# Kernel tuning notes

Hardware: AMD Instinct MI355X
Metric: run time of the kernel (lower is better)

The kernel has to match this reference:

```python
import jax, jax.numpy as jnp
import numpy as np

EPS = 1e-5
NUM_GROUPS = 32


def group_norm(x, scale, bias):
    # x: [B, C, H, W]; normalize over (C//G, H, W) within each of G groups
    B, C, H, W = x.shape
    g = x.reshape(B, NUM_GROUPS, C // NUM_GROUPS, H, W)
    mean = g.mean(axis=(2, 3, 4), keepdims=True)
    var = g.var(axis=(2, 3, 4), keepdims=True)
    g = (g - mean) * jax.lax.rsqrt(var + EPS)
    g = g.reshape(B, C, H, W)
    return g * scale[None, :, None, None] + bias[None, :, None, None]


def conv1x1(x, w, b):
    # x: [B, C, H, W], w: [Cout, Cin], b: [Cout]
    return jnp.einsum('bchw,oc->bohw', x, w) + b[None, :, None, None]


def setup_inputs() -> dict:
    key = jax.random.key(0)
    ks = jax.random.split(key, 8)
    B, C, H, W = 8, 256, 64, 64
    xavier = (6.0 / (C + C)) ** 0.5
    inp = {
        'x': jax.random.normal(ks[0], (B, C, H, W), jnp.float32),
        'target': jax.random.normal(ks[1], (B, C, H, W), jnp.float32),
        'gn_scale': jnp.ones((C,), jnp.float32),
        'gn_bias': jnp.zeros((C,), jnp.float32),
        'Wq': jax.random.uniform(ks[2], (C, C), jnp.float32, -xavier, xavier),
        'bq': jnp.zeros((C,), jnp.float32),
        'Wk': jax.random.uniform(ks[3], (C, C), jnp.float32, -xavier, xavier),
        'bk': jnp.zeros((C,), jnp.float32),
        'Wv': jax.random.uniform(ks[4], (C, C), jnp.float32, -xavier, xavier),
        'bv': jnp.zeros((C,), jnp.float32),
        'Wp': jax.random.uniform(ks[5], (C, C), jnp.float32, -xavier, xavier) * 1e-05,
        'bp': jnp.zeros((C,), jnp.float32),
    }
    return inp


def reference(x, target, gn_scale, gn_bias, Wq, bq, Wk, bk, Wv, bv, Wp, bp):
    B, C, H, W = x.shape
    hx = group_norm(x, gn_scale, gn_bias)
    hy = group_norm(target, gn_scale, gn_bias)
    q = conv1x1(hx, Wq, bq)  # [B,C,H,W]
    k = conv1x1(hy, Wk, bk)
    v = conv1x1(hy, Wv, bv)
    q = q.transpose(0, 2, 3, 1).reshape(B, H * W, C)  # [B,HW,C]
    k = k.reshape(B, C, H * W)                         # [B,C,HW]
    w = jnp.einsum('bnc,bcm->bnm', q, k) * (C ** -0.5)  # [B,HW,HW]
    w = jax.nn.softmax(w, axis=-1)
    v = v.transpose(0, 2, 3, 1).reshape(B, H * W, C)   # [B,HW,C]
    h = jnp.einsum('bnm,bmc->bnc', w, v)               # [B,HW,C]
    h = h.reshape(B, H, W, C).transpose(0, 3, 1, 2)    # [B,C,H,W]
    return conv1x1(h, Wp, bp)
```

## Files before the change

### kernel.cpp

```cpp
#include <hip/hip_runtime.h>
#include <cstdint>
#include <cstddef>

typedef _Float16 f16;
typedef _Float16 half8 __attribute__((ext_vector_type(8)));
typedef float floatx4 __attribute__((ext_vector_type(4)));

#define B_ 8
#define C_ 256
#define HW_ 4096
#define EPS_ 1e-5f
#define KVB 32
#define DEFER_THR 8.0f
#define WP_S 65536.0f
#define WP_I (1.0f / 65536.0f)

__device__ __forceinline__ floatx4 mfma16(half8 a, half8 b, floatx4 c) {
  return __builtin_amdgcn_mfma_f32_16x16x32_f16(a, b, c, 0, 0, 0);
}

__global__ void gn_stats(const float* __restrict__ x, const float* __restrict__ y,
                         float* __restrict__ stats) {
  int bid = blockIdx.x;
  int which = bid >> 8;
  int b = (bid >> 5) & 7;
  int g = bid & 31;
  const float* src = which ? y : x;
  const float* base = src + ((size_t)b * C_ + (size_t)g * 8) * HW_;
  float s = 0.f, ss = 0.f;
  const float4* base4 = (const float4*)base;
  for (int i = threadIdx.x; i < 8 * HW_ / 4; i += 256) {
    float4 v = base4[i];
    s += v.x + v.y + v.z + v.w;
    ss += v.x * v.x + v.y * v.y + v.z * v.z + v.w * v.w;
  }
#pragma unroll
  for (int m = 1; m <= 32; m <<= 1) { s += __shfl_xor(s, m); ss += __shfl_xor(ss, m); }
  __shared__ float red[8];
  int wv = threadIdx.x >> 6;
  if ((threadIdx.x & 63) == 0) { red[wv] = s; red[4 + wv] = ss; }
  __syncthreads();
  if (threadIdx.x == 0) {
    float S = red[0] + red[1] + red[2] + red[3];
    float SS = red[4] + red[5] + red[6] + red[7];
    float mean = S / 32768.f;
    float var = SS / 32768.f - mean * mean;
    stats[bid * 2 + 0] = mean;
    stats[bid * 2 + 1] = rsqrtf(var + EPS_);
  }
}

__global__ void gn_apply(const float* __restrict__ x, const float* __restrict__ y,
                         const float* __restrict__ stats,
                         const float* __restrict__ gsc, const float* __restrict__ gbi,
                         f16* __restrict__ hx, f16* __restrict__ hy) {
  int bid = blockIdx.x;
  int which = bid >> 10;
  int b = (bid >> 7) & 7;
  int hw0 = (bid & 127) * 32;
  const float* src = which ? y : x;
  f16* dst = which ? hy : hx;
  const float* st = stats + which * (B_ * 32 * 2);
  int hw = threadIdx.x & 31;
  int c0 = (threadIdx.x >> 5) * 32;
  uint4 ob[4];
  f16* buf = (f16*)ob;
#pragma unroll
  for (int cc = 0; cc < 32; ++cc) {
    int c = c0 + cc;
    int g = c >> 3;
    float mean = st[(b * 32 + g) * 2 + 0];
    float rstd = st[(b * 32 + g) * 2 + 1];
    float v = src[((size_t)b * C_ + c) * HW_ + hw0 + hw];
    v = (v - mean) * rstd * gsc[c] + gbi[c];
    buf[cc] = (f16)v;
  }
  uint4* o4 = (uint4*)(dst + ((size_t)b * HW_ + hw0 + hw) * C_ + c0);
  o4[0] = ob[0]; o4[1] = ob[1]; o4[2] = ob[2]; o4[3] = ob[3];
}

__global__ void w2h(const float* __restrict__ wq, const float* __restrict__ wk,
                    const float* __restrict__ wv, const float* __restrict__ wp,
                    f16* __restrict__ o) {
  int i = blockIdx.x * 256 + threadIdx.x;
  int m = i >> 16, r = i & 65535;
  float v = (m == 0) ? wq[r] : (m == 1) ? wk[r] : (m == 2) ? wv[r] : wp[r] * WP_S;
  o[i] = (f16)v;
}

template<int BIASM, int OUT>
__global__ __launch_bounds__(256, 2) void gemmh(
    const f16* __restrict__ A, const f16* __restrict__ Bp,
    const float* __restrict__ bias, void* __restrict__ Cout,
    int N, float alpha, long sA, long sB, long sC) {
  __shared__ f16 at[64][264];
  __shared__ f16 bt[64][264];
  int z = blockIdx.z;
  const f16* Ab = A + (size_t)z * sA;
  const f16* Bb = Bp + (size_t)z * sB;
  int bm = blockIdx.x * 64, bn = blockIdx.y * 64;
  int t = threadIdx.x;
  int lane = t & 63, wv = t >> 6, l15 = lane & 15, koff = (lane >> 4) * 8;
  {
    int row = t >> 2, c0 = (t & 3) * 64;
    const uint4* pa = (const uint4*)(Ab + (size_t)(bm + row) * 256 + c0);
    const uint4* pb = (const uint4*)(Bb + (size_t)(bn + row) * 256 + c0);
    uint4* da = (uint4*)&at[row][c0];
    uint4* db = (uint4*)&bt[row][c0];
#pragma unroll
    for (int u = 0; u < 8; ++u) da[u] = pa[u];
#pragma unroll
    for (int u = 0; u < 8; ++u) db[u] = pb[u];
  }
  __syncthreads();
  floatx4 acc[4];
#pragma unroll
  for (int nt = 0; nt < 4; ++nt) acc[nt] = (floatx4){0.f, 0.f, 0.f, 0.f};
#pragma unroll
  for (int kk = 0; kk < 256; kk += 32) {
    half8 a = *(const half8*)&at[wv * 16 + l15][kk + koff];
#pragma unroll
    for (int nt = 0; nt < 4; ++nt) {
      half8 b = *(const half8*)&bt[nt * 16 + l15][kk + koff];
      acc[nt] = mfma16(a, b, acc[nt]);
    }
  }
#pragma unroll
  for (int nt = 0; nt < 4; ++nt) {
    int n = bn + nt * 16 + l15;
#pragma unroll
    for (int r = 0; r < 4; ++r) {
      int m = bm + wv * 16 + (lane >> 4) * 4 + r;
      float bv = bias[BIASM ? m : n];
      size_t idx = (size_t)z * sC + (size_t)m * N + n;
      if (OUT == 0) ((float*)Cout)[idx] = acc[nt][r] * alpha + bv;
      else          ((f16*)Cout)[idx] = (f16)((acc[nt][r] + bv) * alpha);
    }
  }
}

__global__ __launch_bounds__(512, 1) void flashf(
    const f16* __restrict__ Q, const f16* __restrict__ K,
    const f16* __restrict__ V, f16* __restrict__ Hh) {
  int flat = blockIdx.x;
  int b = flat & 7;
  int m0 = (flat >> 3) * 128;
  int t = threadIdx.x;
  int lane = t & 63;
  int wv = t >> 6;
  int l15 = lane & 15;
  int koff = (lane >> 4) * 8;
  const f16* Qb = Q + (size_t)b * HW_ * C_;
  const f16* Kb = K + (size_t)b * HW_ * C_;
  const f16* Vb = V + (size_t)b * C_ * HW_;

  __shared__ f16 ks[2][32][264];
  __shared__ f16 vs[2][256][40];
  __shared__ f16 ps[8][16][40];

  int mrow = m0 + wv * 16 + l15;
  half8 qf[8];
#pragma unroll
  for (int kk = 0; kk < 8; ++kk)
    qf[kk] = *(const half8*)(Qb + (size_t)mrow * C_ + kk * 32 + koff);

  floatx4 o[16];
#pragma unroll
  for (int i = 0; i < 16; ++i) o[i] = (floatx4){0.f, 0.f, 0.f, 0.f};
  floatx4 osum = (floatx4){0.f, 0.f, 0.f, 0.f};
  float m_run[4] = {-1e30f, -1e30f, -1e30f, -1e30f};

  int krow = t >> 4, kch = (t & 15) * 16;
  int vrow = t >> 1, vch = (t & 1) * 16;
  uint4 rk0, rk1, rv0, rv1;

#define LOADT(N0)                                                            \
  {                                                                          \
    const uint4* pk = (const uint4*)(Kb + (size_t)((N0) + krow) * C_ + kch); \
    rk0 = pk[0]; rk1 = pk[1];                                                \
    const uint4* pv = (const uint4*)(Vb + (size_t)vrow * HW_ + (N0) + vch);  \
    rv0 = pv[0]; rv1 = pv[1];                                                \
  }
#define STORET(BUF)                                                          \
  {                                                                          \
    uint4* dk = (uint4*)&ks[BUF][krow][kch];                                 \
    dk[0] = rk0; dk[1] = rk1;                                                \
    uint4* dv = (uint4*)&vs[BUF][vrow][vch];                                 \
    dv[0] = rv0; dv[1] = rv1;                                                \
  }

  LOADT(0);
  STORET(0);
  LOADT(KVB);
  __syncthreads();

  const half8 ones = {(f16)1, (f16)1, (f16)1, (f16)1,
                      (f16)1, (f16)1, (f16)1, (f16)1};

  int cur = 0;
  for (int n0 = 0; n0 < HW_; n0 += KVB) {
    floatx4 s0 = {0.f, 0.f, 0.f, 0.f};
    floatx4 s1 = {0.f, 0.f, 0.f, 0.f};
    __builtin_amdgcn_s_setprio(1);
#pragma unroll
    for (int kk = 0; kk < 8; ++kk) {
      half8 k0 = *(const half8*)&ks[cur][l15][kk * 32 + koff];
      half8 k1 = *(const half8*)&ks[cur][16 + l15][kk * 32 + koff];
      s0 = mfma16(qf[kk], k0, s0);
      s1 = mfma16(qf[kk], k1, s1);
    }
    __builtin_amdgcn_s_setprio(0);

    int trig = 0;
#pragma unroll
    for (int r = 0; r < 4; ++r) {
      float thr = m_run[r] + DEFER_THR;
      trig |= (s0[r] > thr) | (s1[r] > thr);
    }
    if (__any(trig)) {
      float sc[4];
#pragma unroll
      for (int r = 0; r < 4; ++r) {
        float tm = fmaxf(s0[r], s1[r]);
        tm = fmaxf(tm, __shfl_xor(tm, 1));
        tm = fmaxf(tm, __shfl_xor(tm, 2));
        tm = fmaxf(tm, __shfl_xor(tm, 4));
        tm = fmaxf(tm, __shfl_xor(tm, 8));
        float mn = fmaxf(m_run[r], tm);
        sc[r] = __expf(m_run[r] - mn);
        m_run[r] = mn;
      }
      osum[0] *= sc[0]; osum[1] *= sc[1]; osum[2] *= sc[2]; osum[3] *= sc[3];
#pragma unroll
      for (int i = 0; i < 16; ++i) {
        o[i][0] *= sc[0]; o[i][1] *= sc[1]; o[i][2] *= sc[2]; o[i][3] *= sc[3];
      }
    }
#pragma unroll
    for (int r = 0; r < 4; ++r) {
      float p0 = __expf(s0[r] - m_run[r]);
      float p1 = __expf(s1[r] - m_run[r]);
      int mr = (lane >> 4) * 4 + r;
      ps[wv][mr][l15] = (f16)p0;
      ps[wv][mr][16 + l15] = (f16)p1;
    }
    asm volatile("s_waitcnt lgkmcnt(0)" ::: "memory");
    __builtin_amdgcn_sched_barrier(0);
    half8 pf = *(const half8*)&ps[wv][l15][koff];
    __builtin_amdgcn_s_setprio(1);
#pragma unroll
    for (int ct = 0; ct < 16; ++ct) {
      half8 vf = *(const half8*)&vs[cur][ct * 16 + l15][koff];
      o[ct] = mfma16(pf, vf, o[ct]);
    }
    osum = mfma16(pf, ones, osum);
    __builtin_amdgcn_s_setprio(0);

    bool h1 = n0 + KVB < HW_;
    bool h2 = n0 + 2 * KVB < HW_;
    if (h1) STORET(cur ^ 1);
    if (h2) LOADT(n0 + 2 * KVB);
    __syncthreads();
    cur ^= 1;
  }

  float inv[4];
#pragma unroll
  for (int r = 0; r < 4; ++r) inv[r] = 1.f / osum[r];
#pragma unroll
  for (int ct = 0; ct < 16; ++ct) {
#pragma unroll
    for (int r = 0; r < 4; ++r) {
      int m = m0 + wv * 16 + (lane >> 4) * 4 + r;
      Hh[((size_t)b * HW_ + m) * C_ + ct * 16 + l15] = (f16)(o[ct][r] * inv[r]);
    }
  }
#undef LOADT
#undef STORET
}

extern "C" void kernel_launch(void* const* d_in, const int* in_sizes, int n_in,
                              void* d_out, int out_size, void* d_ws, size_t ws_size,
                              hipStream_t stream) {
  const float* x   = (const float*)d_in[0];
  const float* tg  = (const float*)d_in[1];
  const float* gsc = (const float*)d_in[2];
  const float* gbi = (const float*)d_in[3];
  const float* Wq  = (const float*)d_in[4];
  const float* bq  = (const float*)d_in[5];
  const float* Wk  = (const float*)d_in[6];
  const float* bk  = (const float*)d_in[7];
  const float* Wv  = (const float*)d_in[8];
  const float* bv  = (const float*)d_in[9];
  const float* Wp  = (const float*)d_in[10];
  const float* bp  = (const float*)d_in[11];

  char* ws = (char*)d_ws;
  size_t off = 0;
  auto alloc = [&](size_t bytes) {
    char* p = ws + off;
    off += (bytes + 255) & ~(size_t)255;
    return p;
  };
  const size_t HSZ = (size_t)B_ * HW_ * C_ * sizeof(f16);
  f16* hx = (f16*)alloc(HSZ);
  f16* hy = (f16*)alloc(HSZ);
  f16* qh = (f16*)alloc(HSZ);
  f16* kh = (f16*)alloc(HSZ);
  f16* vh = (f16*)alloc(HSZ);
  f16* hh = (f16*)alloc(HSZ);
  f16* w16 = (f16*)alloc((size_t)4 * 65536 * sizeof(f16));
  float* stats = (float*)alloc((size_t)2 * B_ * 32 * 2 * sizeof(float));

  gn_stats<<<dim3(512), dim3(256), 0, stream>>>(x, tg, stats);
  gn_apply<<<dim3(2048), dim3(256), 0, stream>>>(x, tg, stats, gsc, gbi, hx, hy);
  w2h<<<dim3(1024), dim3(256), 0, stream>>>(Wq, Wk, Wv, Wp, w16);
  f16* wq16 = w16;
  f16* wk16 = w16 + 65536;
  f16* wv16 = w16 + 2 * 65536;
  f16* wp16 = w16 + 3 * 65536;

  const long sT = (long)HW_ * C_;

  gemmh<0, 1><<<dim3(512, 4, 1), dim3(256), 0, stream>>>(
      hx, wq16, bq, qh, C_, 0.0625f, 0L, 0L, 0L);
  gemmh<0, 1><<<dim3(512, 4, 1), dim3(256), 0, stream>>>(
      hy, wk16, bk, kh, C_, 1.f, 0L, 0L, 0L);
  gemmh<1, 1><<<dim3(4, 64, 8), dim3(256), 0, stream>>>(
      wv16, hy, bv, vh, HW_, 1.f, 0L, sT, (long)C_ * HW_);
  flashf<<<dim3(256), dim3(512), 0, stream>>>(qh, kh, vh, hh);
  gemmh<1, 0><<<dim3(4, 64, 8), dim3(256), 0, stream>>>(
      wp16, hh, bp, d_out, HW_, WP_I, 0L, sT, (long)C_ * HW_);
}
```

Measured before the change: 322.8 us.

## Rewrite flash attention with 32x32x16 MFMA and transposed S, register-resident P

The attention kernel now uses 32x32x16 MFMA tiles with 4 waves of 32 query rows each, computing S transposed (K as A operand) so each lane owns one query column. The softmax probabilities go straight into MFMA operands through packed fp16 conversion and cross-half shuffles, so the LDS round-trip for P goes away. Row sums are kept in a scalar running value instead of an extra ones-MFMA. K shared memory uses an XOR swizzle in place of padding. The goal is fewer LDS transactions and higher MFMA efficiency, at the cost of more registers and half the waves per block.

```diff
diff --git a/kernel.cpp b/kernel.cpp
--- a/kernel.cpp
+++ b/kernel.cpp
@@ -4,7 +4,9 @@
 
 typedef _Float16 f16;
 typedef _Float16 half8 __attribute__((ext_vector_type(8)));
+typedef __fp16 fp16x2 __attribute__((ext_vector_type(2)));
 typedef float floatx4 __attribute__((ext_vector_type(4)));
+typedef float floatx16 __attribute__((ext_vector_type(16)));
 
 #define B_ 8
 #define C_ 256
@@ -17,6 +19,9 @@
 
 __device__ __forceinline__ floatx4 mfma16(half8 a, half8 b, floatx4 c) {
   return __builtin_amdgcn_mfma_f32_16x16x32_f16(a, b, c, 0, 0, 0);
+}
+__device__ __forceinline__ floatx16 mfma32(half8 a, half8 b, floatx16 c) {
+  return __builtin_amdgcn_mfma_f32_32x32x16_f16(a, b, c, 0, 0, 0);
 }
 
 __global__ void gn_stats(const float* __restrict__ x, const float* __restrict__ y,
@@ -139,7 +144,7 @@
   }
 }
 
-__global__ __launch_bounds__(512, 1) void flashf(
+__global__ __launch_bounds__(256, 1) void flash32x(
     const f16* __restrict__ Q, const f16* __restrict__ K,
     const f16* __restrict__ V, f16* __restrict__ Hh) {
   int flat = blockIdx.x;
@@ -148,45 +153,51 @@
   int t = threadIdx.x;
   int lane = t & 63;
   int wv = t >> 6;
-  int l15 = lane & 15;
-  int koff = (lane >> 4) * 8;
+  int l31 = lane & 31;
+  int h = lane >> 5;
   const f16* Qb = Q + (size_t)b * HW_ * C_;
   const f16* Kb = K + (size_t)b * HW_ * C_;
   const f16* Vb = V + (size_t)b * C_ * HW_;
 
-  __shared__ f16 ks[2][32][264];
+  __shared__ f16 ks[2][32 * 256];
   __shared__ f16 vs[2][256][40];
-  __shared__ f16 ps[8][16][40];
-
-  int mrow = m0 + wv * 16 + l15;
-  half8 qf[8];
-#pragma unroll
-  for (int kk = 0; kk < 8; ++kk)
-    qf[kk] = *(const half8*)(Qb + (size_t)mrow * C_ + kk * 32 + koff);
-
-  floatx4 o[16];
-#pragma unroll
-  for (int i = 0; i < 16; ++i) o[i] = (floatx4){0.f, 0.f, 0.f, 0.f};
-  floatx4 osum = (floatx4){0.f, 0.f, 0.f, 0.f};
-  float m_run[4] = {-1e30f, -1e30f, -1e30f, -1e30f};
-
-  int krow = t >> 4, kch = (t & 15) * 16;
-  int vrow = t >> 1, vch = (t & 1) * 16;
-  uint4 rk0, rk1, rv0, rv1;
-
-#define LOADT(N0)                                                            \
-  {                                                                          \
-    const uint4* pk = (const uint4*)(Kb + (size_t)((N0) + krow) * C_ + kch); \
-    rk0 = pk[0]; rk1 = pk[1];                                                \
-    const uint4* pv = (const uint4*)(Vb + (size_t)vrow * HW_ + (N0) + vch);  \
-    rv0 = pv[0]; rv1 = pv[1];                                                \
-  }
-#define STORET(BUF)                                                          \
-  {                                                                          \
-    uint4* dk = (uint4*)&ks[BUF][krow][kch];                                 \
-    dk[0] = rk0; dk[1] = rk1;                                                \
-    uint4* dv = (uint4*)&vs[BUF][vrow][vch];                                 \
-    dv[0] = rv0; dv[1] = rv1;                                                \
+  __shared__ float lbc[4][32];
+
+  int qrow = m0 + wv * 32 + l31;
+  half8 qf[16];
+#pragma unroll
+  for (int kk = 0; kk < 16; ++kk)
+    qf[kk] = *(const half8*)(Qb + (size_t)qrow * C_ + kk * 16 + h * 8);
+
+  floatx16 o[8];
+#pragma unroll
+  for (int ct = 0; ct < 8; ++ct)
+#pragma unroll
+    for (int r = 0; r < 16; ++r) o[ct][r] = 0.f;
+  float m_run = -1e30f, l_run = 0.f;
+
+  int krow = t >> 3, kc0 = (t & 7) * 4;
+  int vr = t >> 1, vc = (t & 1) * 16;
+  uint4 rk[4], rv[4];
+
+#define LOADT(N0)                                                              \
+  {                                                                            \
+    const uint4* pk = (const uint4*)(Kb + (size_t)((N0) + krow) * C_ + kc0 * 8); \
+    rk[0] = pk[0]; rk[1] = pk[1]; rk[2] = pk[2]; rk[3] = pk[3];                \
+    const uint4* pv0 = (const uint4*)(Vb + (size_t)vr * HW_ + (N0) + vc);      \
+    rv[0] = pv0[0]; rv[1] = pv0[1];                                            \
+    const uint4* pv1 = (const uint4*)(Vb + (size_t)(vr + 128) * HW_ + (N0) + vc); \
+    rv[2] = pv1[0]; rv[3] = pv1[1];                                            \
+  }
+#define STORET(BUF)                                                            \
+  {                                                                            \
+    _Pragma("unroll")                                                          \
+    for (int u = 0; u < 4; ++u)                                                \
+      *(uint4*)&ks[BUF][krow * 256 + (((kc0 + u) ^ (krow & 7)) << 3)] = rk[u]; \
+    *(uint4*)&vs[BUF][vr][vc] = rv[0];                                         \
+    *(uint4*)&vs[BUF][vr][vc + 8] = rv[1];                                     \
+    *(uint4*)&vs[BUF][vr + 128][vc] = rv[2];                                   \
+    *(uint4*)&vs[BUF][vr + 128][vc + 8] = rv[3];                               \
   }
 
   LOADT(0);
@@ -194,66 +205,68 @@
   LOADT(KVB);
   __syncthreads();
 
-  const half8 ones = {(f16)1, (f16)1, (f16)1, (f16)1,
-                      (f16)1, (f16)1, (f16)1, (f16)1};
-
   int cur = 0;
   for (int n0 = 0; n0 < HW_; n0 += KVB) {
-    floatx4 s0 = {0.f, 0.f, 0.f, 0.f};
-    floatx4 s1 = {0.f, 0.f, 0.f, 0.f};
+    floatx16 st;
+#pragma unroll
+    for (int r = 0; r < 16; ++r) st[r] = 0.f;
     __builtin_amdgcn_s_setprio(1);
 #pragma unroll
-    for (int kk = 0; kk < 8; ++kk) {
-      half8 k0 = *(const half8*)&ks[cur][l15][kk * 32 + koff];
-      half8 k1 = *(const half8*)&ks[cur][16 + l15][kk * 32 + koff];
-      s0 = mfma16(qf[kk], k0, s0);
-      s1 = mfma16(qf[kk], k1, s1);
+    for (int kk = 0; kk < 16; ++kk) {
+      half8 kf = *(const half8*)&ks[cur][(l31 << 8) + (((2 * kk + h) ^ (l31 & 7)) << 3)];
+      st = mfma32(kf, qf[kk], st);
     }
     __builtin_amdgcn_s_setprio(0);
 
-    int trig = 0;
-#pragma unroll
-    for (int r = 0; r < 4; ++r) {
-      float thr = m_run[r] + DEFER_THR;
-      trig |= (s0[r] > thr) | (s1[r] > thr);
-    }
+    float m16 = st[0];
+#pragma unroll
+    for (int r = 1; r < 16; ++r) m16 = fmaxf(m16, st[r]);
+    float mf = fmaxf(m16, __shfl_xor(m16, 32));
+    int trig = mf > m_run + DEFER_THR;
     if (__any(trig)) {
-      float sc[4];
-#pragma unroll
-      for (int r = 0; r < 4; ++r) {
-        float tm = fmaxf(s0[r], s1[r]);
-        tm = fmaxf(tm, __shfl_xor(tm, 1));
-        tm = fmaxf(tm, __shfl_xor(tm, 2));
-        tm = fmaxf(tm, __shfl_xor(tm, 4));
-        tm = fmaxf(tm, __shfl_xor(tm, 8));
-        float mn = fmaxf(m_run[r], tm);
-        sc[r] = __expf(m_run[r] - mn);
-        m_run[r] = mn;
+      float mn = fmaxf(m_run, mf);
+      float sc = __expf(m_run - mn);
+      m_run = mn;
+      l_run *= sc;
+      if (lane < 32) lbc[wv][l31] = sc;
+      asm volatile("s_waitcnt lgkmcnt(0)" ::: "memory");
+      __builtin_amdgcn_sched_barrier(0);
+#pragma unroll
+      for (int r = 0; r < 16; ++r) {
+        float scr = lbc[wv][(r & 3) + 8 * (r >> 2) + 4 * h];
+#pragma unroll
+        for (int ct = 0; ct < 8; ++ct) o[ct][r] *= scr;
       }
-      osum[0] *= sc[0]; osum[1] *= sc[1]; osum[2] *= sc[2]; osum[3] *= sc[3];
-#pragma unroll
-      for (int i = 0; i < 16; ++i) {
-        o[i][0] *= sc[0]; o[i][1] *= sc[1]; o[i][2] *= sc[2]; o[i][3] *= sc[3];
-      }
-    }
-#pragma unroll
-    for (int r = 0; r < 4; ++r) {
-      float p0 = __expf(s0[r] - m_run[r]);
-      float p1 = __expf(s1[r] - m_run[r]);
-      int mr = (lane >> 4) * 4 + r;
-      ps[wv][mr][l15] = (f16)p0;
-      ps[wv][mr][16 + l15] = (f16)p1;
-    }
-    asm volatile("s_waitcnt lgkmcnt(0)" ::: "memory");
-    __builtin_amdgcn_sched_barrier(0);
-    half8 pf = *(const half8*)&ps[wv][l15][koff];
+    }
+    float p[16];
+    float part = 0.f;
+#pragma unroll
+    for (int r = 0; r < 16; ++r) { p[r] = __expf(st[r] - m_run); part += p[r]; }
+    l_run += part + __shfl_xor(part, 32);
+
+    unsigned w[8];
+#pragma unroll
+    for (int j = 0; j < 8; ++j) {
+      fp16x2 pk2 = __builtin_amdgcn_cvt_pkrtz(p[2 * j], p[2 * j + 1]);
+      w[j] = __builtin_bit_cast(unsigned, pk2);
+    }
+    unsigned sw[8];
+#pragma unroll
+    for (int j = 0; j < 8; ++j) sw[j] = (unsigned)__shfl_xor((int)w[j], 32);
+    union { unsigned u[4]; half8 v; } f1, f2;
+    f1.u[0] = h ? sw[2] : w[0]; f1.u[1] = h ? sw[3] : w[1];
+    f1.u[2] = h ? w[2] : sw[0]; f1.u[3] = h ? w[3] : sw[1];
+    f2.u[0] = h ? sw[6] : w[4]; f2.u[1] = h ? sw[7] : w[5];
+    f2.u[2] = h ? w[6] : sw[4]; f2.u[3] = h ? w[7] : sw[5];
+
     __builtin_amdgcn_s_setprio(1);
 #pragma unroll
-    for (int ct = 0; ct < 16; ++ct) {
-      half8 vf = *(const half8*)&vs[cur][ct * 16 + l15][koff];
-      o[ct] = mfma16(pf, vf, o[ct]);
-    }
-    osum = mfma16(pf, ones, osum);
+    for (int ct = 0; ct < 8; ++ct) {
+      half8 v0 = *(const half8*)&vs[cur][ct * 32 + l31][h * 8];
+      half8 v1 = *(const half8*)&vs[cur][ct * 32 + l31][16 + h * 8];
+      o[ct] = mfma32(f1.v, v0, o[ct]);
+      o[ct] = mfma32(f2.v, v1, o[ct]);
+    }
     __builtin_amdgcn_s_setprio(0);
 
     bool h1 = n0 + KVB < HW_;
@@ -264,16 +277,16 @@
     cur ^= 1;
   }
 
-  float inv[4];
-#pragma unroll
-  for (int r = 0; r < 4; ++r) inv[r] = 1.f / osum[r];
-#pragma unroll
-  for (int ct = 0; ct < 16; ++ct) {
-#pragma unroll
-    for (int r = 0; r < 4; ++r) {
-      int m = m0 + wv * 16 + (lane >> 4) * 4 + r;
-      Hh[((size_t)b * HW_ + m) * C_ + ct * 16 + l15] = (f16)(o[ct][r] * inv[r]);
-    }
+  if (lane < 32) lbc[wv][l31] = 1.f / l_run;
+  asm volatile("s_waitcnt lgkmcnt(0)" ::: "memory");
+  __builtin_amdgcn_sched_barrier(0);
+#pragma unroll
+  for (int r = 0; r < 16; ++r) {
+    float li = lbc[wv][(r & 3) + 8 * (r >> 2) + 4 * h];
+    int q = m0 + wv * 32 + (r & 3) + 8 * (r >> 2) + 4 * h;
+#pragma unroll
+    for (int ct = 0; ct < 8; ++ct)
+      Hh[((size_t)b * HW_ + q) * C_ + ct * 32 + l31] = (f16)(o[ct][r] * li);
   }
 #undef LOADT
 #undef STORET
@@ -328,7 +341,7 @@
       hy, wk16, bk, kh, C_, 1.f, 0L, 0L, 0L);
   gemmh<1, 1><<<dim3(4, 64, 8), dim3(256), 0, stream>>>(
       wv16, hy, bv, vh, HW_, 1.f, 0L, sT, (long)C_ * HW_);
-  flashf<<<dim3(256), dim3(512), 0, stream>>>(qh, kh, vh, hh);
+  flash32x<<<dim3(256), dim3(256), 0, stream>>>(qh, kh, vh, hh);
   gemmh<1, 0><<<dim3(4, 64, 8), dim3(256), 0, stream>>>(
       wp16, hh, bp, d_out, HW_, WP_I, 0L, sT, (long)C_ * HW_);
 }
```

Measured after the change: 523.0 us. +62.0%, slower.

## Split attention KV range in two halves and merge partials in a combine kernel

Applied to the files above, without the earlier changes.

The attention kernel now launches twice as many blocks, each handling half of the 4096 keys/values for a 128-query tile. Each block writes unnormalized fp32 partial outputs plus per-row running max and sum. A new combine kernel rescales and merges the two halves into the f16 attention output. The aim is more parallelism and occupancy on the GPU. The cost is extra fp32 partial-output traffic and one additional launch. The V shared-memory tile padding also shrinks from 40 to 36, with 8-byte stores and loads, which changes the LDS bank pattern.

```diff
diff --git a/kernel.cpp b/kernel.cpp
--- a/kernel.cpp
+++ b/kernel.cpp
@@ -17,6 +17,13 @@
 
 __device__ __forceinline__ floatx4 mfma16(half8 a, half8 b, floatx4 c) {
   return __builtin_amdgcn_mfma_f32_16x16x32_f16(a, b, c, 0, 0, 0);
+}
+
+__device__ __forceinline__ half8 ld8u2(const f16* p) {
+  union { uint2 u[2]; half8 h; } t;
+  t.u[0] = *(const uint2*)p;
+  t.u[1] = *(const uint2*)(p + 4);
+  return t.h;
 }
 
 __global__ void gn_stats(const float* __restrict__ x, const float* __restrict__ y,
@@ -139,12 +146,15 @@
   }
 }
 
-__global__ __launch_bounds__(512, 1) void flashf(
+__global__ __launch_bounds__(512, 1) void flashp16(
     const f16* __restrict__ Q, const f16* __restrict__ K,
-    const f16* __restrict__ V, f16* __restrict__ Hh) {
+    const f16* __restrict__ V, float* __restrict__ op0,
+    float* __restrict__ op1, float2* __restrict__ ml) {
   int flat = blockIdx.x;
   int b = flat & 7;
-  int m0 = (flat >> 3) * 128;
+  int u = flat >> 3;
+  int m0 = (u & 31) * 128;
+  int half = u >> 5;
   int t = threadIdx.x;
   int lane = t & 63;
   int wv = t >> 6;
@@ -153,9 +163,11 @@
   const f16* Qb = Q + (size_t)b * HW_ * C_;
   const f16* Kb = K + (size_t)b * HW_ * C_;
   const f16* Vb = V + (size_t)b * C_ * HW_;
+  float* op = half ? op1 : op0;
+  const int kvb = half * 2048;
 
   __shared__ f16 ks[2][32][264];
-  __shared__ f16 vs[2][256][40];
+  __shared__ f16 vs[2][256][36];
   __shared__ f16 ps[8][16][40];
 
   int mrow = m0 + wv * 16 + l15;
@@ -171,34 +183,38 @@
   float m_run[4] = {-1e30f, -1e30f, -1e30f, -1e30f};
 
   int krow = t >> 4, kch = (t & 15) * 16;
-  int vrow = t >> 1, vch = (t & 1) * 16;
+  int vr = t >> 1, vc = (t & 1) * 16;
   uint4 rk0, rk1, rv0, rv1;
 
-#define LOADT(N0)                                                            \
+#define LOADT(TI)                                                            \
   {                                                                          \
-    const uint4* pk = (const uint4*)(Kb + (size_t)((N0) + krow) * C_ + kch); \
+    int n0 = kvb + (TI) * KVB;                                               \
+    const uint4* pk = (const uint4*)(Kb + (size_t)(n0 + krow) * C_ + kch);   \
     rk0 = pk[0]; rk1 = pk[1];                                                \
-    const uint4* pv = (const uint4*)(Vb + (size_t)vrow * HW_ + (N0) + vch);  \
+    const uint4* pv = (const uint4*)(Vb + (size_t)vr * HW_ + n0 + vc);       \
     rv0 = pv[0]; rv1 = pv[1];                                                \
   }
 #define STORET(BUF)                                                          \
   {                                                                          \
     uint4* dk = (uint4*)&ks[BUF][krow][kch];                                 \
     dk[0] = rk0; dk[1] = rk1;                                                \
-    uint4* dv = (uint4*)&vs[BUF][vrow][vch];                                 \
-    dv[0] = rv0; dv[1] = rv1;                                                \
+    f16* dv = &vs[BUF][vr][vc];                                              \
+    *(uint2*)(dv + 0)  = make_uint2(rv0.x, rv0.y);                           \
+    *(uint2*)(dv + 4)  = make_uint2(rv0.z, rv0.w);                           \
+    *(uint2*)(dv + 8)  = make_uint2(rv1.x, rv1.y);                           \
+    *(uint2*)(dv + 12) = make_uint2(rv1.z, rv1.w);                           \
   }
 
   LOADT(0);
   STORET(0);
-  LOADT(KVB);
+  LOADT(1);
   __syncthreads();
 
   const half8 ones = {(f16)1, (f16)1, (f16)1, (f16)1,
                       (f16)1, (f16)1, (f16)1, (f16)1};
 
   int cur = 0;
-  for (int n0 = 0; n0 < HW_; n0 += KVB) {
+  for (int ti = 0; ti < 64; ++ti) {
     floatx4 s0 = {0.f, 0.f, 0.f, 0.f};
     floatx4 s1 = {0.f, 0.f, 0.f, 0.f};
     __builtin_amdgcn_s_setprio(1);
@@ -250,33 +266,62 @@
     __builtin_amdgcn_s_setprio(1);
 #pragma unroll
     for (int ct = 0; ct < 16; ++ct) {
-      half8 vf = *(const half8*)&vs[cur][ct * 16 + l15][koff];
+      half8 vf = ld8u2(&vs[cur][ct * 16 + l15][koff]);
       o[ct] = mfma16(pf, vf, o[ct]);
     }
     osum = mfma16(pf, ones, osum);
     __builtin_amdgcn_s_setprio(0);
 
-    bool h1 = n0 + KVB < HW_;
-    bool h2 = n0 + 2 * KVB < HW_;
-    if (h1) STORET(cur ^ 1);
-    if (h2) LOADT(n0 + 2 * KVB);
+    if (ti + 1 < 64) STORET(cur ^ 1);
+    if (ti + 2 < 64) LOADT(ti + 2);
     __syncthreads();
     cur ^= 1;
   }
 
-  float inv[4];
-#pragma unroll
-  for (int r = 0; r < 4; ++r) inv[r] = 1.f / osum[r];
+  if (l15 == 0) {
+#pragma unroll
+    for (int r = 0; r < 4; ++r) {
+      int q = m0 + wv * 16 + (lane >> 4) * 4 + r;
+      ml[(size_t)half * (B_ * HW_) + (size_t)b * HW_ + q] =
+          make_float2(m_run[r], osum[r]);
+    }
+  }
 #pragma unroll
   for (int ct = 0; ct < 16; ++ct) {
 #pragma unroll
     for (int r = 0; r < 4; ++r) {
       int m = m0 + wv * 16 + (lane >> 4) * 4 + r;
-      Hh[((size_t)b * HW_ + m) * C_ + ct * 16 + l15] = (f16)(o[ct][r] * inv[r]);
+      op[((size_t)b * HW_ + m) * C_ + ct * 16 + l15] = o[ct][r];
     }
   }
 #undef LOADT
 #undef STORET
+}
+
+__global__ __launch_bounds__(256) void fcomb(
+    const float* __restrict__ op0, const float* __restrict__ op1,
+    const float2* __restrict__ ml, f16* __restrict__ hh) {
+  int t = threadIdx.x;
+  int row = blockIdx.x * 32 + (t >> 3);
+  int c0 = (t & 7) * 32;
+  float2 a = ml[row];
+  float2 bq = ml[B_ * HW_ + row];
+  float mm = fmaxf(a.x, bq.x);
+  float e1 = __expf(a.x - mm), e2 = __expf(bq.x - mm);
+  float inv = 1.f / (a.y * e1 + bq.y * e2);
+  float f1 = e1 * inv, f2 = e2 * inv;
+  size_t base = (size_t)row * C_ + c0;
+#pragma unroll
+  for (int j = 0; j < 8; ++j) {
+    float4 x = *(const float4*)&op0[base + j * 4];
+    float4 y = *(const float4*)&op1[base + j * 4];
+    f16 outv[4];
+    outv[0] = (f16)(x.x * f1 + y.x * f2);
+    outv[1] = (f16)(x.y * f1 + y.y * f2);
+    outv[2] = (f16)(x.z * f1 + y.z * f2);
+    outv[3] = (f16)(x.w * f1 + y.w * f2);
+    *(uint2*)&hh[base + j * 4] = *(uint2*)outv;
+  }
 }
 
 extern "C" void kernel_launch(void* const* d_in, const int* in_sizes, int n_in,
@@ -309,8 +354,11 @@
   f16* kh = (f16*)alloc(HSZ);
   f16* vh = (f16*)alloc(HSZ);
   f16* hh = (f16*)alloc(HSZ);
+  float* op1 = (float*)alloc((size_t)B_ * HW_ * C_ * sizeof(float));
+  float2* ml = (float2*)alloc((size_t)2 * B_ * HW_ * sizeof(float2));
   f16* w16 = (f16*)alloc((size_t)4 * 65536 * sizeof(f16));
   float* stats = (float*)alloc((size_t)2 * B_ * 32 * 2 * sizeof(float));
+  float* op0 = (float*)hx;
 
   gn_stats<<<dim3(512), dim3(256), 0, stream>>>(x, tg, stats);
   gn_apply<<<dim3(2048), dim3(256), 0, stream>>>(x, tg, stats, gsc, gbi, hx, hy);
@@ -328,7 +376,8 @@
       hy, wk16, bk, kh, C_, 1.f, 0L, 0L, 0L);
   gemmh<1, 1><<<dim3(4, 64, 8), dim3(256), 0, stream>>>(
       wv16, hy, bv, vh, HW_, 1.f, 0L, sT, (long)C_ * HW_);
-  flashf<<<dim3(256), dim3(512), 0, stream>>>(qh, kh, vh, hh);
+  flashp16<<<dim3(512), dim3(512), 0, stream>>>(qh, kh, vh, op0, op1, ml);
+  fcomb<<<dim3(1024), dim3(256), 0, stream>>>(op0, op1, ml, hh);
   gemmh<1, 0><<<dim3(4, 64, 8), dim3(256), 0, stream>>>(
       wp16, hh, bp, d_out, HW_, WP_I, 0L, sT, (long)C_ * HW_);
 }
```

Result: slower. 342.7 us (+6.2%).
